# Performance work log

Hardware: AMD Instinct MI355X
Metric: run time of the kernel (lower is better)

## Reference

```python
import jax, jax.numpy as jnp
import numpy as np

N_NODES = 100000
N_EDGES = 1600000
DIM = 3
HID = 128
BN_EPS = 1e-5


def _bn(x, g, b):
    # BatchNorm1d, training-mode batch statistics (biased variance, like torch)
    m = jnp.mean(x, axis=0)
    v = jnp.var(x, axis=0)
    return (x - m) * jax.lax.rsqrt(v + BN_EPS) * g + b


def _gin_mlp(h, w1, b1, g1, be1, w2, b2, g2, be2, w3, b3):
    # Linear -> BN -> ReLU -> (Dropout: identity in eval) -> Linear -> BN -> ReLU -> Linear
    h = jax.nn.relu(_bn(h @ w1 + b1, g1, be1))
    h = jax.nn.relu(_bn(h @ w2 + b2, g2, be2))
    return h @ w3 + b3


def _gin_conv(x, src, dst, eps, mlp_params):
    # GINConv: mlp((1+eps)*x_i + sum_{j->i} x_j); scatter-add over edge targets
    agg = jax.ops.segment_sum(x[src], dst, num_segments=N_NODES)
    return _gin_mlp((1.0 + eps) * x + agg, *mlp_params)


def setup_inputs() -> dict:
    key = jax.random.key(0)
    ks = jax.random.split(key, 32)

    def w(k, shape, scale=0.05):
        return jax.random.normal(k, shape, dtype=jnp.float32) * scale

    inp = {}
    inp["coords"] = jax.random.normal(ks[0], (N_NODES, DIM), dtype=jnp.float32)
    inp["edge_index"] = jax.random.randint(ks[1], (2, N_EDGES), 0, N_NODES, dtype=jnp.int32)

    # GIN layer 0 MLP (dim -> hid -> hid -> hid)
    inp["g0_w1"] = w(ks[2], (DIM, HID)); inp["g0_b1"] = jnp.zeros((HID,), jnp.float32)
    inp["g0_g1"] = jnp.ones((HID,), jnp.float32); inp["g0_be1"] = jnp.zeros((HID,), jnp.float32)
    inp["g0_w2"] = w(ks[3], (HID, HID)); inp["g0_b2"] = jnp.zeros((HID,), jnp.float32)
    inp["g0_g2"] = jnp.ones((HID,), jnp.float32); inp["g0_be2"] = jnp.zeros((HID,), jnp.float32)
    inp["g0_w3"] = w(ks[4], (HID, HID)); inp["g0_b3"] = jnp.zeros((HID,), jnp.float32)
    inp["eps0"] = jnp.zeros((), jnp.float32)
    inp["bn0_g"] = jnp.ones((HID,), jnp.float32); inp["bn0_b"] = jnp.zeros((HID,), jnp.float32)

    # GIN layer 1 MLP (hid -> hid -> hid -> hid)
    inp["g1_w1"] = w(ks[5], (HID, HID)); inp["g1_b1"] = jnp.zeros((HID,), jnp.float32)
    inp["g1_g1"] = jnp.ones((HID,), jnp.float32); inp["g1_be1"] = jnp.zeros((HID,), jnp.float32)
    inp["g1_w2"] = w(ks[6], (HID, HID)); inp["g1_b2"] = jnp.zeros((HID,), jnp.float32)
    inp["g1_g2"] = jnp.ones((HID,), jnp.float32); inp["g1_be2"] = jnp.zeros((HID,), jnp.float32)
    inp["g1_w3"] = w(ks[7], (HID, HID)); inp["g1_b3"] = jnp.zeros((HID,), jnp.float32)
    inp["eps1"] = jnp.zeros((), jnp.float32)
    inp["bn1_g"] = jnp.ones((HID,), jnp.float32); inp["bn1_b"] = jnp.zeros((HID,), jnp.float32)

    # decoder MLP: (2*hid+1) -> hid -> hid//2 -> 1, sigmoid
    inp["d_w1"] = w(ks[8], (2 * HID + 1, HID)); inp["d_b1"] = jnp.zeros((HID,), jnp.float32)
    inp["d_g"] = jnp.ones((HID,), jnp.float32); inp["d_be"] = jnp.zeros((HID,), jnp.float32)
    inp["d_w2"] = w(ks[9], (HID, HID // 2)); inp["d_b2"] = jnp.zeros((HID // 2,), jnp.float32)
    inp["d_w3"] = w(ks[10], (HID // 2, 1)); inp["d_b3"] = jnp.zeros((1,), jnp.float32)
    return inp


def reference(coords, edge_index,
              g0_w1, g0_b1, g0_g1, g0_be1, g0_w2, g0_b2, g0_g2, g0_be2, g0_w3, g0_b3, eps0, bn0_g, bn0_b,
              g1_w1, g1_b1, g1_g1, g1_be1, g1_w2, g1_b2, g1_g2, g1_be2, g1_w3, g1_b3, eps1, bn1_g, bn1_b,
              d_w1, d_b1, d_g, d_be, d_w2, d_b2, d_w3, d_b3):
    node_0 = edge_index[0]
    node_1 = edge_index[1]

    mlp0 = (g0_w1, g0_b1, g0_g1, g0_be1, g0_w2, g0_b2, g0_g2, g0_be2, g0_w3, g0_b3)
    mlp1 = (g1_w1, g1_b1, g1_g1, g1_be1, g1_w2, g1_b2, g1_g2, g1_be2, g1_w3, g1_b3)

    x = _gin_conv(coords, node_0, node_1, eps0, mlp0)
    x = jax.nn.relu(_bn(x, bn0_g, bn0_b))
    x = _gin_conv(x, node_0, node_1, eps1, mlp1)
    x = jax.nn.relu(_bn(x, bn1_g, bn1_b))

    # edge_l_cntr branch: per-edge contour-length feature + endpoint concat
    l = jnp.linalg.norm(coords[node_1] - coords[node_0], axis=1, keepdims=True)  # [E,1]
    h = jnp.concatenate([x[node_0], x[node_1], l], axis=-1)  # [E, 2*hid+1]

    h = jax.nn.relu(_bn(h @ d_w1 + d_b1, d_g, d_be))
    h = jax.nn.relu(h @ d_w2 + d_b2)
    out = jax.nn.sigmoid((h @ d_w3 + d_b3).squeeze(-1))  # [E]
    return out
```

## Files before the change

kernel.cpp:

```cpp
#include <hip/hip_runtime.h>
#include <hip/hip_bf16.h>
#include <math.h>


typedef __attribute__((ext_vector_type(8))) __bf16 bf16x8;
typedef __attribute__((ext_vector_type(4))) float f32x4;

__device__ __forceinline__ unsigned int pack_bf16(float a, float b) {
    unsigned short ua = __builtin_bit_cast(unsigned short, __float2bfloat16(a));
    unsigned short ub = __builtin_bit_cast(unsigned short, __float2bfloat16(b));
    return (unsigned int)ua | ((unsigned int)ub << 16);
}
__device__ __forceinline__ float bflo(unsigned int u) {
    return __builtin_bit_cast(float, u << 16);
}
__device__ __forceinline__ float bfhi(unsigned int u) {
    return __builtin_bit_cast(float, u & 0xffff0000u);
}


__global__ void hist_dst(const int* __restrict__ edst, int* __restrict__ cursor, int E) {
    int e = blockIdx.x * 256 + threadIdx.x;
    if (e < E) atomicAdd(&cursor[edst[e]], 1);
}

__global__ __launch_bounds__(1024) void scan_deg(const int* deg, int* rowoff, int* cursor, int N) {
    __shared__ int sums[1024];
    const int t = threadIdx.x;
    const int chunk = (N + 1023) >> 10;
    int lo = t * chunk, hi = lo + chunk;
    if (lo > N) lo = N;
    if (hi > N) hi = N;
    int s = 0;
    for (int i = lo; i < hi; ++i) s += deg[i];
    sums[t] = s;
    __syncthreads();
    for (int off = 1; off < 1024; off <<= 1) {
        int add = (t >= off) ? sums[t - off] : 0;
        __syncthreads();
        sums[t] += add;
        __syncthreads();
    }
    int run = sums[t] - s;
    for (int i = lo; i < hi; ++i) {
        int d = deg[i];
        rowoff[i] = run;
        cursor[i] = run;
        run += d;
    }
    if (t == 1023) rowoff[N] = sums[1023];
}

__global__ void fill_csr(const int* __restrict__ esrc, const int* __restrict__ edst,
                         const float* __restrict__ coords,
                         int* cursor, int* __restrict__ perm, int* __restrict__ dperm,
                         int* __restrict__ eperm, float* __restrict__ lperm, int E) {
    int e = blockIdx.x * 256 + threadIdx.x;
    if (e >= E) return;
    int s0 = esrc[e], d0 = edst[e];
    int pos = atomicAdd(&cursor[d0], 1);
    perm[pos] = s0;
    dperm[pos] = d0;
    eperm[pos] = e;
    float dx = coords[d0*3+0] - coords[s0*3+0];
    float dy = coords[d0*3+1] - coords[s0*3+1];
    float dz = coords[d0*3+2] - coords[s0*3+2];
    lperm[pos] = sqrtf(dx*dx + dy*dy + dz*dz);
}


__global__ void gather_coords(const float* __restrict__ coords,
                              const int* __restrict__ rowoff, const int* __restrict__ perm,
                              float* __restrict__ agg0, int N) {
    int i = blockIdx.x * 256 + threadIdx.x;
    if (i >= N) return;
    float ax = 0.f, ay = 0.f, az = 0.f;
    int b = rowoff[i], t = rowoff[i+1];
    for (int j = b; j < t; ++j) {
        int p = perm[j];
        ax += coords[p*3+0];
        ay += coords[p*3+1];
        az += coords[p*3+2];
    }
    agg0[i*3+0] = ax; agg0[i*3+1] = ay; agg0[i*3+2] = az;
}

__global__ __launch_bounds__(256) void gather_combine_bn(const float* __restrict__ x,
                                                         const int* __restrict__ rowoff,
                                                         const int* __restrict__ perm,
                                                         const float* __restrict__ st,
                                                         const float* __restrict__ g,
                                                         const float* __restrict__ be,
                                                         float invN,
                                                         const float* __restrict__ eps,
                                                         float* __restrict__ y, int N) {
    int node = blockIdx.x * 4 + (threadIdx.x >> 6);
    int lane = threadIdx.x & 63;
    if (node >= N) return;
    float ep = 1.f + *eps;
    int c0 = lane*2, c1 = c0 + 1;
    float m0 = st[c0]*invN, m1 = st[c1]*invN;
    float v0 = fmaxf(st[128+c0]*invN - m0*m0, 0.f);
    float v1 = fmaxf(st[128+c1]*invN - m1*m1, 0.f);
    float a0 = g[c0]*rsqrtf(v0 + 1e-5f), a1 = g[c1]*rsqrtf(v1 + 1e-5f);
    float2 scv = make_float2(a0, a1);
    float2 shv = make_float2(be[c0] - m0*a0, be[c1] - m1*a1);
    const float2* x2 = (const float2*)x;
    int b = rowoff[node], t = rowoff[node+1];
    float2 acc = make_float2(0.f, 0.f);
    int j = b;
    for (; j + 2 <= t; j += 2) {
        int p0 = perm[j], p1 = perm[j+1];
        float2 v0v = x2[(size_t)p0*64 + lane];
        float2 v1v = x2[(size_t)p1*64 + lane];
        acc.x += fmaxf(fmaf(v0v.x, scv.x, shv.x), 0.f) + fmaxf(fmaf(v1v.x, scv.x, shv.x), 0.f);
        acc.y += fmaxf(fmaf(v0v.y, scv.y, shv.y), 0.f) + fmaxf(fmaf(v1v.y, scv.y, shv.y), 0.f);
    }
    if (j < t) {
        int p = perm[j];
        float2 v = x2[(size_t)p*64 + lane];
        acc.x += fmaxf(fmaf(v.x, scv.x, shv.x), 0.f);
        acc.y += fmaxf(fmaf(v.y, scv.y, shv.y), 0.f);
    }
    float2 own = x2[(size_t)node*64 + lane];
    acc.x = fmaf(ep, fmaxf(fmaf(own.x, scv.x, shv.x), 0.f), acc.x);
    acc.y = fmaf(ep, fmaxf(fmaf(own.y, scv.y, shv.y), 0.f), acc.y);
    ((float2*)y)[(size_t)node*64 + lane] = acc;
}


__global__ __launch_bounds__(256) void lin0(const float* __restrict__ coords,
                                            const float* __restrict__ agg0,
                                            const float* __restrict__ W1,
                                            const float* __restrict__ b1,
                                            const float* __restrict__ eps0,
                                            float* __restrict__ t1,
                                            float* __restrict__ stats, int nrows) {
    int col = threadIdx.x & 127, half = threadIdx.x >> 7;
    float w0 = W1[col], w1 = W1[128+col], w2 = W1[256+col], bb = b1[col];
    float ep = 1.f + *eps0;
    float s = 0.f, q = 0.f;
    int r0 = blockIdx.x * 64;
    for (int i = 0; i < 32; ++i) {
        int row = r0 + half + 2*i;
        if (row < nrows) {
            float h0 = fmaf(ep, coords[row*3+0], agg0[row*3+0]);
            float h1 = fmaf(ep, coords[row*3+1], agg0[row*3+1]);
            float h2 = fmaf(ep, coords[row*3+2], agg0[row*3+2]);
            float v = fmaf(h0, w0, fmaf(h1, w1, fmaf(h2, w2, bb)));
            t1[row*128+col] = v;
            s += v; q += v*v;
        }
    }
    __shared__ float red[512];
    red[half*128+col] = s;
    red[256 + half*128+col] = q;
    __syncthreads();
    if (threadIdx.x < 128) {
        atomicAdd(&stats[col],       red[col] + red[128+col]);
        atomicAdd(&stats[128+col],   red[256+col] + red[384+col]);
    }
}

__global__ void prep_w2(const float* __restrict__ W2, unsigned short* __restrict__ w2t) {
    int i = blockIdx.x * 256 + threadIdx.x;
    if (i >= 128*64) return;
    int k = i >> 6, c = i & 63;
    w2t[c*128 + k] = __builtin_bit_cast(unsigned short, __float2bfloat16(W2[i]));
}

__global__ void prep_wT(const float* __restrict__ w0, const float* __restrict__ w1,
                        const float* __restrict__ w2, const float* __restrict__ w3,
                        const float* __restrict__ w4, const float* __restrict__ w5,
                        const float* __restrict__ w6, unsigned short* __restrict__ dst) {
    int m = blockIdx.y;
    const float* src = (m==0)?w0:(m==1)?w1:(m==2)?w2:(m==3)?w3:(m==4)?w4:(m==5)?w5:w6;
    int i = blockIdx.x * 256 + threadIdx.x;
    int k = i >> 7, c = i & 127;
    dst[m*16384 + c*128 + k] =
        __builtin_bit_cast(unsigned short, __float2bfloat16(src[i]));
}

template<bool IN_BN, bool STATS, bool OUT_BF16>
__global__ __launch_bounds__(256) void gemm_mfma(const float* __restrict__ A,
                                                 const unsigned short* __restrict__ wT,
                                                 const float* __restrict__ bias,
                                                 const float* __restrict__ inst,
                                                 const float* __restrict__ bng,
                                                 const float* __restrict__ bnb,
                                                 float invCnt,
                                                 float* __restrict__ C,
                                                 unsigned short* __restrict__ Cb,
                                                 float* __restrict__ stats, int nrows) {
    __shared__ int4 sAi[1024];
    __shared__ int4 sBi[2048];
    __shared__ float sred[2][4][128];
    char* sA = (char*)sAi;
    char* sB = (char*)sBi;
    float* sSC = &sred[0][0][0];
    float* sSH = &sred[0][1][0];
    const int tid = threadIdx.x;
    const int tile0 = blockIdx.x * 64;

    if (IN_BN) {
        if (tid < 128) {
            float m = inst[tid] * invCnt;
            float v = fmaxf(inst[128+tid] * invCnt - m*m, 0.f);
            float a = bng[tid] * rsqrtf(v + 1e-5f);
            sSC[tid] = a;
            sSH[tid] = bnb[tid] - m*a;
        }
        __syncthreads();
    }

    {
        const int4* src = (const int4*)wT;
        #pragma unroll
        for (int ii = 0; ii < 8; ++ii) {
            int s = tid + 256*ii;
            int col = s >> 4, k16 = s & 15;
            int byte = ((col << 8) + (k16 << 4)) ^ ((col & 7) << 4);
            *(int4*)(sB + byte) = src[s];
        }
    }
    {
        const int c4 = tid & 31;
        const int rb = tid >> 5;
        float4 s4, t4;
        if (IN_BN) {
            s4 = ((const float4*)sSC)[c4];
            t4 = ((const float4*)sSH)[c4];
        }
        const float4* A4 = (const float4*)A;
        #pragma unroll
        for (int i = 0; i < 8; ++i) {
            int r = rb + 8*i;
            int row = tile0 + r;
            float4 v = make_float4(0.f, 0.f, 0.f, 0.f);
            if (row < nrows) {
                v = A4[(size_t)row*32 + c4];
                if (IN_BN) {
                    v.x = fmaxf(fmaf(v.x, s4.x, t4.x), 0.f);
                    v.y = fmaxf(fmaf(v.y, s4.y, t4.y), 0.f);
                    v.z = fmaxf(fmaf(v.z, s4.z, t4.z), 0.f);
                    v.w = fmaxf(fmaf(v.w, s4.w, t4.w), 0.f);
                }
            }
            uint2 pk;
            pk.x = pack_bf16(v.x, v.y);
            pk.y = pack_bf16(v.z, v.w);
            int byte = ((r << 8) + (c4 << 3)) ^ ((r & 7) << 4);
            *(uint2*)(sA + byte) = pk;
        }
    }
    __syncthreads();

    const int l = tid & 63;
    const int w = tid >> 6;
    const int arow = (w << 4) + (l & 15);
    const int kbase = (l >> 4) << 3;
    f32x4 accv[8];
    #pragma unroll
    for (int c = 0; c < 8; ++c) accv[c] = (f32x4){0.f, 0.f, 0.f, 0.f};

    #pragma unroll
    for (int t = 0; t < 4; ++t) {
        int k0 = t*32 + kbase;
        int abyte = ((arow << 8) + (k0 << 1)) ^ ((arow & 7) << 4);
        bf16x8 af = __builtin_bit_cast(bf16x8, *(const int4*)(sA + abyte));
        #pragma unroll
        for (int c = 0; c < 8; ++c) {
            int bcol = (c << 4) + (l & 15);
            int bbyte = ((bcol << 8) + (k0 << 1)) ^ ((bcol & 7) << 4);
            bf16x8 bf = __builtin_bit_cast(bf16x8, *(const int4*)(sB + bbyte));
            accv[c] = __builtin_amdgcn_mfma_f32_16x16x32_bf16(af, bf, accv[c], 0, 0, 0);
        }
    }

    const int rj = (l >> 4) << 2;
    float lsum[8], lsq[8];
    #pragma unroll
    for (int c = 0; c < 8; ++c) {
        int col = (c << 4) + (l & 15);
        float bv = bias ? bias[col] : 0.f;
        f32x4 a = accv[c];
        float s = 0.f, q = 0.f;
        #pragma unroll
        for (int j = 0; j < 4; ++j) {
            int row = tile0 + (w << 4) + rj + j;
            float o = a[j] + bv;
            if (row < nrows) {
                if (OUT_BF16)
                    Cb[(size_t)row*128 + col] =
                        __builtin_bit_cast(unsigned short, __float2bfloat16(o));
                else
                    C[(size_t)row*128 + col] = o;
                if (STATS) { s += o; q += o*o; }
            }
        }
        lsum[c] = s; lsq[c] = q;
    }
    if (STATS) {
        #pragma unroll
        for (int c = 0; c < 8; ++c) {
            lsum[c] += __shfl_xor(lsum[c], 16, 64);
            lsum[c] += __shfl_xor(lsum[c], 32, 64);
            lsq[c]  += __shfl_xor(lsq[c], 16, 64);
            lsq[c]  += __shfl_xor(lsq[c], 32, 64);
        }
        __syncthreads();
        if ((l >> 4) == 0) {
            #pragma unroll
            for (int c = 0; c < 8; ++c) {
                int col = (c << 4) + l;
                sred[0][w][col] = lsum[c];
                sred[1][w][col] = lsq[c];
            }
        }
        __syncthreads();
        if (tid < 128) {
            float s = sred[0][0][tid] + sred[0][1][tid] + sred[0][2][tid] + sred[0][3][tid];
            float q = sred[1][0][tid] + sred[1][1][tid] + sred[1][2][tid] + sred[1][3][tid];
            atomicAdd(&stats[tid], s);
            atomicAdd(&stats[128 + tid], q);
        }
    }
}

__global__ __launch_bounds__(256) void csr_stats(const unsigned short* __restrict__ ya,
                                                 const unsigned short* __restrict__ yb,
                                                 const int* __restrict__ rowoff,
                                                 const int* __restrict__ perm,
                                                 const float* __restrict__ lperm,
                                                 const float* __restrict__ wl,
                                                 const float* __restrict__ b1,
                                                 float* __restrict__ stats, int N, int nspan) {
    int w = blockIdx.x * 4 + (threadIdx.x >> 6);
    int lane = threadIdx.x & 63;
    const unsigned int* ya2 = (const unsigned int*)ya;
    const unsigned int* yb2 = (const unsigned int*)yb;
    float2 wl2 = ((const float2*)wl)[lane];
    float2 b12 = ((const float2*)b1)[lane];
    float2 s = make_float2(0.f, 0.f), q = make_float2(0.f, 0.f);
    int i0 = w * nspan;
    int i1 = i0 + nspan; if (i1 > N) i1 = N;
    for (int i = i0; i < i1; ++i) {
        unsigned int ub = yb2[(size_t)i*64 + lane];
        float ybx = bflo(ub), yby = bfhi(ub);
        int b = rowoff[i], t = rowoff[i+1];
        for (int j = b; j < t; ++j) {
            int p = perm[j];
            float lv = lperm[j];
            unsigned int ua = ya2[(size_t)p*64 + lane];
            float zx = bflo(ua) + ybx + fmaf(lv, wl2.x, b12.x);
            float zy = bfhi(ua) + yby + fmaf(lv, wl2.y, b12.y);
            s.x += zx; s.y += zy;
            q.x += zx*zx; q.y += zy*zy;
        }
    }
    __shared__ float red[1024];
    int wv = threadIdx.x >> 6;
    red[wv*128 + lane*2]       = s.x;
    red[wv*128 + lane*2 + 1]   = s.y;
    red[512 + wv*128 + lane*2]     = q.x;
    red[512 + wv*128 + lane*2 + 1] = q.y;
    __syncthreads();
    if (threadIdx.x < 128) {
        int c = threadIdx.x;
        float ss = red[c] + red[128+c] + red[256+c] + red[384+c];
        float qq = red[512+c] + red[640+c] + red[768+c] + red[896+c];
        atomicAdd(&stats[c], ss);
        atomicAdd(&stats[128+c], qq);
    }
}

__global__ __launch_bounds__(256) void decoder_fused(const unsigned short* __restrict__ ya,
                                                     const unsigned short* __restrict__ yb,
                                                     const float* __restrict__ lperm,
                                                     const int* __restrict__ perm,
                                                     const int* __restrict__ dperm,
                                                     const int* __restrict__ eperm,
                                                     const float* __restrict__ wl,
                                                     const float* __restrict__ b1,
                                                     const float* __restrict__ st6,
                                                     const float* __restrict__ dg,
                                                     const float* __restrict__ dbe,
                                                     float invE,
                                                     const unsigned short* __restrict__ w2t,
                                                     const float* __restrict__ b2,
                                                     const float* __restrict__ w3,
                                                     const float* __restrict__ b3p,
                                                     float* __restrict__ out, int E) {
    __shared__ int4 sAB[2048];
    char* sA = (char*)sAB;
    char* sB = (char*)sAB + 16384;
    const int tid = threadIdx.x;
    const int tile0 = blockIdx.x * 64;

    {
        const int4* src = (const int4*)w2t;
        #pragma unroll
        for (int ii = 0; ii < 4; ++ii) {
            int s = tid + 256*ii;
            int col = s >> 4, k16 = s & 15;
            int byte = ((col << 8) + (k16 << 4)) ^ ((col & 7) << 4);
            *(int4*)(sB + byte) = src[s];
        }
    }
    {
        const int c4 = tid & 31;
        const int rb = tid >> 5;
        float4 wv = ((const float4*)wl)[c4];
        float4 bb = ((const float4*)b1)[c4];
        float4 s4, t4;
        {
            int cb = c4 * 4;
            #pragma unroll
            for (int j = 0; j < 4; ++j) {
                float m = st6[cb+j] * invE;
                float v = fmaxf(st6[128+cb+j] * invE - m*m, 0.f);
                float a = dg[cb+j] * rsqrtf(v + 1e-5f);
                ((float*)&s4)[j] = a;
                ((float*)&t4)[j] = dbe[cb+j] - m*a;
            }
        }
        const uint2* ya2 = (const uint2*)ya;
        const uint2* yb2 = (const uint2*)yb;
        #pragma unroll
        for (int i = 0; i < 8; ++i) {
            int r = rb + 8*i;
            int row = tile0 + r;
            float4 v = make_float4(0.f, 0.f, 0.f, 0.f);
            if (row < E) {
                int s0 = perm[row], d0 = dperm[row];
                float lv = lperm[row];
                uint2 ua = ya2[(size_t)s0*32 + c4];
                uint2 ubv = yb2[(size_t)d0*32 + c4];
                float vax = bflo(ua.x), vay = bfhi(ua.x), vaz = bflo(ua.y), vaw = bfhi(ua.y);
                float vbx = bflo(ubv.x), vby = bfhi(ubv.x), vbz = bflo(ubv.y), vbw = bfhi(ubv.y);
                v.x = fmaxf(fmaf(vax + vbx + fmaf(lv, wv.x, bb.x), s4.x, t4.x), 0.f);
                v.y = fmaxf(fmaf(vay + vby + fmaf(lv, wv.y, bb.y), s4.y, t4.y), 0.f);
                v.z = fmaxf(fmaf(vaz + vbz + fmaf(lv, wv.z, bb.z), s4.z, t4.z), 0.f);
                v.w = fmaxf(fmaf(vaw + vbw + fmaf(lv, wv.w, bb.w), s4.w, t4.w), 0.f);
            }
            uint2 pk;
            pk.x = pack_bf16(v.x, v.y);
            pk.y = pack_bf16(v.z, v.w);
            int byte = ((r << 8) + (c4 << 3)) ^ ((r & 7) << 4);
            *(uint2*)(sA + byte) = pk;
        }
    }
    __syncthreads();

    const int l = tid & 63;
    const int w = tid >> 6;
    const int arow = (w << 4) + (l & 15);
    const int kbase = (l >> 4) << 3;
    f32x4 accv[4];
    #pragma unroll
    for (int c = 0; c < 4; ++c) accv[c] = (f32x4){0.f, 0.f, 0.f, 0.f};

    #pragma unroll
    for (int t = 0; t < 4; ++t) {
        int k0 = t*32 + kbase;
        int abyte = ((arow << 8) + (k0 << 1)) ^ ((arow & 7) << 4);
        bf16x8 af = __builtin_bit_cast(bf16x8, *(const int4*)(sA + abyte));
        #pragma unroll
        for (int c = 0; c < 4; ++c) {
            int bcol = (c << 4) + (l & 15);
            int bbyte = ((bcol << 8) + (k0 << 1)) ^ ((bcol & 7) << 4);
            bf16x8 bf = __builtin_bit_cast(bf16x8, *(const int4*)(sB + bbyte));
            accv[c] = __builtin_amdgcn_mfma_f32_16x16x32_bf16(af, bf, accv[c], 0, 0, 0);
        }
    }

    float p0 = 0.f, p1 = 0.f, p2 = 0.f, p3 = 0.f;
    #pragma unroll
    for (int c = 0; c < 4; ++c) {
        int col = (c << 4) + (l & 15);
        float b2c = b2[col], w3c = w3[col];
        f32x4 a = accv[c];
        p0 = fmaf(fmaxf(a[0] + b2c, 0.f), w3c, p0);
        p1 = fmaf(fmaxf(a[1] + b2c, 0.f), w3c, p1);
        p2 = fmaf(fmaxf(a[2] + b2c, 0.f), w3c, p2);
        p3 = fmaf(fmaxf(a[3] + b2c, 0.f), w3c, p3);
    }
    #pragma unroll
    for (int m = 1; m < 16; m <<= 1) {
        p0 += __shfl_xor(p0, m, 64);
        p1 += __shfl_xor(p1, m, 64);
        p2 += __shfl_xor(p2, m, 64);
        p3 += __shfl_xor(p3, m, 64);
    }
    if ((l & 15) == 0) {
        float b3v = b3p[0];
        int rbase = tile0 + (w << 4) + ((l >> 4) << 2);
        float pj[4] = {p0, p1, p2, p3};
        #pragma unroll
        for (int j = 0; j < 4; ++j) {
            int row = rbase + j;
            if (row < E) out[eperm[row]] = 1.f / (1.f + expf(-(pj[j] + b3v)));
        }
    }
}


extern "C" void kernel_launch(void* const* d_in, const int* in_sizes, int n_in,
                              void* d_out, int out_size, void* d_ws, size_t ws_size,
                              hipStream_t stream) {
    const int N = in_sizes[0] / 3;
    const int E = in_sizes[1] / 2;

    const float* coords = (const float*)d_in[0];
    const int*   ei     = (const int*)d_in[1];
    const int*   esrc = ei;
    const int*   edst = ei + E;
    const float* g0_w1 = (const float*)d_in[2];
    const float* g0_b1 = (const float*)d_in[3];
    const float* g0_g1 = (const float*)d_in[4];
    const float* g0_be1= (const float*)d_in[5];
    const float* g0_w2 = (const float*)d_in[6];
    const float* g0_b2 = (const float*)d_in[7];
    const float* g0_g2 = (const float*)d_in[8];
    const float* g0_be2= (const float*)d_in[9];
    const float* g0_w3 = (const float*)d_in[10];
    const float* g0_b3 = (const float*)d_in[11];
    const float* eps0  = (const float*)d_in[12];
    const float* bn0_g = (const float*)d_in[13];
    const float* bn0_b = (const float*)d_in[14];
    const float* g1_w1 = (const float*)d_in[15];
    const float* g1_b1 = (const float*)d_in[16];
    const float* g1_g1 = (const float*)d_in[17];
    const float* g1_be1= (const float*)d_in[18];
    const float* g1_w2 = (const float*)d_in[19];
    const float* g1_b2 = (const float*)d_in[20];
    const float* g1_g2 = (const float*)d_in[21];
    const float* g1_be2= (const float*)d_in[22];
    const float* g1_w3 = (const float*)d_in[23];
    const float* g1_b3 = (const float*)d_in[24];
    const float* eps1  = (const float*)d_in[25];
    const float* bn1_g = (const float*)d_in[26];
    const float* bn1_b = (const float*)d_in[27];
    const float* d_w1  = (const float*)d_in[28];
    const float* d_b1  = (const float*)d_in[29];
    const float* d_g   = (const float*)d_in[30];
    const float* d_be  = (const float*)d_in[31];
    const float* d_w2  = (const float*)d_in[32];
    const float* d_b2  = (const float*)d_in[33];
    const float* d_w3  = (const float*)d_in[34];
    const float* d_b3  = (const float*)d_in[35];

    float* ws = (float*)d_ws;
    const size_t NF = (size_t)N * 128;
    float* buf0 = ws;
    float* buf1 = ws + NF;
    float* buf2 = ws + 2*NF;
    float* agg0 = ws + 3*NF;
    float* stats= agg0 + (size_t)N*3;
    float* scsh = stats + 7*256;
    float* lperm = scsh + 7*256;
    int*   cursor = (int*)(lperm + E);
    int*   rowoff = cursor + N;
    int*   perm   = rowoff + N + 1;
    int*   dperm  = perm + E;
    int*   eperm  = dperm + E;
    unsigned short* w2t = (unsigned short*)(eperm + E);
    unsigned short* wT  = w2t + 64*128;
    unsigned short* ya_bf = (unsigned short*)buf1;
    unsigned short* yb_bf = (unsigned short*)buf2;

    float* out = (float*)d_out;

    const float* wl = d_w1 + 256*128;

    #define STATSK(k) (stats + (k)*256)
    #define WT(m) (wT + (m)*16384)

    const int rowTiles = (N + 63) / 64;
    const int edgeTiles = (E + 63) / 64;
    const int eBlocks = (E + 255) / 256;
    const float invN = 1.f / (float)N;
    const float invE = 1.f / (float)E;
    const int nWaves = 2048 * 4;
    const int nspan = (N + nWaves - 1) / nWaves;

    hipMemsetAsync(stats, 0, 7*256 * sizeof(float), stream);
    hipMemsetAsync(cursor, 0, (size_t)N * sizeof(int), stream);

    hist_dst<<<eBlocks, 256, 0, stream>>>(edst, cursor, E);
    scan_deg<<<1, 1024, 0, stream>>>(cursor, rowoff, cursor, N);
    fill_csr<<<eBlocks, 256, 0, stream>>>(esrc, edst, coords, cursor, perm, dperm, eperm, lperm, E);
    prep_w2<<<32, 256, 0, stream>>>(d_w2, w2t);
    prep_wT<<<dim3(64, 7), 256, 0, stream>>>(g0_w2, g0_w3, g1_w1, g1_w2, g1_w3,
                                             d_w1, d_w1 + 128*128, wT);

    gather_coords<<<(N + 255)/256, 256, 0, stream>>>(coords, rowoff, perm, agg0, N);
    lin0<<<rowTiles, 256, 0, stream>>>(coords, agg0, g0_w1, g0_b1, eps0, buf0, STATSK(0), N);
    gemm_mfma<true,true,false><<<rowTiles, 256, 0, stream>>>(
        buf0, WT(0), g0_b2, STATSK(0), g0_g1, g0_be1, invN, buf1, nullptr, STATSK(1), N);
    gemm_mfma<true,true,false><<<rowTiles, 256, 0, stream>>>(
        buf1, WT(1), g0_b3, STATSK(1), g0_g2, g0_be2, invN, buf2, nullptr, STATSK(2), N);

    gather_combine_bn<<<(N + 3)/4, 256, 0, stream>>>(
        buf2, rowoff, perm, STATSK(2), bn0_g, bn0_b, invN, eps1, buf0, N);
    gemm_mfma<false,true,false><<<rowTiles, 256, 0, stream>>>(
        buf0, WT(2), g1_b1, nullptr, nullptr, nullptr, 0.f, buf1, nullptr, STATSK(3), N);
    gemm_mfma<true,true,false><<<rowTiles, 256, 0, stream>>>(
        buf1, WT(3), g1_b2, STATSK(3), g1_g1, g1_be1, invN, buf2, nullptr, STATSK(4), N);
    gemm_mfma<true,true,false><<<rowTiles, 256, 0, stream>>>(
        buf2, WT(4), g1_b3, STATSK(4), g1_g2, g1_be2, invN, buf0, nullptr, STATSK(5), N);

    gemm_mfma<true,false,true><<<rowTiles, 256, 0, stream>>>(
        buf0, WT(5), nullptr, STATSK(5), bn1_g, bn1_b, invN, nullptr, ya_bf, nullptr, N);
    gemm_mfma<true,false,true><<<rowTiles, 256, 0, stream>>>(
        buf0, WT(6), nullptr, STATSK(5), bn1_g, bn1_b, invN, nullptr, yb_bf, nullptr, N);
    csr_stats<<<2048, 256, 0, stream>>>(ya_bf, yb_bf, rowoff, perm, lperm, wl, d_b1,
                                        STATSK(6), N, nspan);
    decoder_fused<<<edgeTiles, 256, 0, stream>>>(ya_bf, yb_bf, lperm, perm, dperm, eperm,
                                                 wl, d_b1, STATSK(6), d_g, d_be, invE,
                                                 w2t, d_b2, d_w3, d_b3, out, E);
}
```

Baseline: 1.512 ms.

## Store node activations as bf16 and make decoder a persistent grid-stride kernel

All intermediate node feature buffers (lin0 output, GEMM outputs, gather_combine_bn input and output) now hold bf16 instead of fp32, which halves the memory traffic of the gather and GEMM stages. The GEMM A-tile load now reads packed bf16 int4 vectors and applies BN+ReLU on the unpacked values. Separately, the decoder now runs on a fixed grid of 1280 blocks that loop over edge tiles, so the w2t weight tile is loaded into shared memory once per block instead of once per tile. The risk is extra rounding error from storing pre-BN activations in bf16, while BN statistics are still accumulated from the fp32 values.

New measurement: 1.500 ms. Within noise of the previous version (-0.7%).

```diff
diff --git a/kernel.cpp b/kernel.cpp
--- a/kernel.cpp
+++ b/kernel.cpp
@@ -16,6 +16,9 @@
 }
 __device__ __forceinline__ float bfhi(unsigned int u) {
     return __builtin_bit_cast(float, u & 0xffff0000u);
+}
+__device__ __forceinline__ unsigned short bf16r(float a) {
+    return __builtin_bit_cast(unsigned short, __float2bfloat16(a));
 }
 
 
@@ -85,7 +88,7 @@
     agg0[i*3+0] = ax; agg0[i*3+1] = ay; agg0[i*3+2] = az;
 }
 
-__global__ __launch_bounds__(256) void gather_combine_bn(const float* __restrict__ x,
+__global__ __launch_bounds__(256) void gather_combine_bn(const unsigned short* __restrict__ x,
                                                          const int* __restrict__ rowoff,
                                                          const int* __restrict__ perm,
                                                          const float* __restrict__ st,
@@ -93,7 +96,7 @@
                                                          const float* __restrict__ be,
                                                          float invN,
                                                          const float* __restrict__ eps,
-                                                         float* __restrict__ y, int N) {
+                                                         unsigned short* __restrict__ y, int N) {
     int node = blockIdx.x * 4 + (threadIdx.x >> 6);
     int lane = threadIdx.x & 63;
     if (node >= N) return;
@@ -103,29 +106,27 @@
     float v0 = fmaxf(st[128+c0]*invN - m0*m0, 0.f);
     float v1 = fmaxf(st[128+c1]*invN - m1*m1, 0.f);
     float a0 = g[c0]*rsqrtf(v0 + 1e-5f), a1 = g[c1]*rsqrtf(v1 + 1e-5f);
-    float2 scv = make_float2(a0, a1);
-    float2 shv = make_float2(be[c0] - m0*a0, be[c1] - m1*a1);
-    const float2* x2 = (const float2*)x;
+    float sx = a0, sy = a1;
+    float hx = be[c0] - m0*a0, hy = be[c1] - m1*a1;
+    const unsigned int* x2 = (const unsigned int*)x;
     int b = rowoff[node], t = rowoff[node+1];
-    float2 acc = make_float2(0.f, 0.f);
+    float accx = 0.f, accy = 0.f;
     int j = b;
     for (; j + 2 <= t; j += 2) {
-        int p0 = perm[j], p1 = perm[j+1];
-        float2 v0v = x2[(size_t)p0*64 + lane];
-        float2 v1v = x2[(size_t)p1*64 + lane];
-        acc.x += fmaxf(fmaf(v0v.x, scv.x, shv.x), 0.f) + fmaxf(fmaf(v1v.x, scv.x, shv.x), 0.f);
-        acc.y += fmaxf(fmaf(v0v.y, scv.y, shv.y), 0.f) + fmaxf(fmaf(v1v.y, scv.y, shv.y), 0.f);
+        unsigned int u0 = x2[(size_t)perm[j]*64 + lane];
+        unsigned int u1 = x2[(size_t)perm[j+1]*64 + lane];
+        accx += fmaxf(fmaf(bflo(u0), sx, hx), 0.f) + fmaxf(fmaf(bflo(u1), sx, hx), 0.f);
+        accy += fmaxf(fmaf(bfhi(u0), sy, hy), 0.f) + fmaxf(fmaf(bfhi(u1), sy, hy), 0.f);
     }
     if (j < t) {
-        int p = perm[j];
-        float2 v = x2[(size_t)p*64 + lane];
-        acc.x += fmaxf(fmaf(v.x, scv.x, shv.x), 0.f);
-        acc.y += fmaxf(fmaf(v.y, scv.y, shv.y), 0.f);
-    }
-    float2 own = x2[(size_t)node*64 + lane];
-    acc.x = fmaf(ep, fmaxf(fmaf(own.x, scv.x, shv.x), 0.f), acc.x);
-    acc.y = fmaf(ep, fmaxf(fmaf(own.y, scv.y, shv.y), 0.f), acc.y);
-    ((float2*)y)[(size_t)node*64 + lane] = acc;
+        unsigned int u = x2[(size_t)perm[j]*64 + lane];
+        accx += fmaxf(fmaf(bflo(u), sx, hx), 0.f);
+        accy += fmaxf(fmaf(bfhi(u), sy, hy), 0.f);
+    }
+    unsigned int uo = x2[(size_t)node*64 + lane];
+    accx = fmaf(ep, fmaxf(fmaf(bflo(uo), sx, hx), 0.f), accx);
+    accy = fmaf(ep, fmaxf(fmaf(bfhi(uo), sy, hy), 0.f), accy);
+    ((unsigned int*)y)[(size_t)node*64 + lane] = pack_bf16(accx, accy);
 }
 
 
@@ -134,7 +135,7 @@
                                             const float* __restrict__ W1,
                                             const float* __restrict__ b1,
                                             const float* __restrict__ eps0,
-                                            float* __restrict__ t1,
+                                            unsigned short* __restrict__ t1,
                                             float* __restrict__ stats, int nrows) {
     int col = threadIdx.x & 127, half = threadIdx.x >> 7;
     float w0 = W1[col], w1 = W1[128+col], w2 = W1[256+col], bb = b1[col];
@@ -148,7 +149,7 @@
             float h1 = fmaf(ep, coords[row*3+1], agg0[row*3+1]);
             float h2 = fmaf(ep, coords[row*3+2], agg0[row*3+2]);
             float v = fmaf(h0, w0, fmaf(h1, w1, fmaf(h2, w2, bb)));
-            t1[row*128+col] = v;
+            t1[row*128+col] = bf16r(v);
             s += v; q += v*v;
         }
     }
@@ -166,7 +167,7 @@
     int i = blockIdx.x * 256 + threadIdx.x;
     if (i >= 128*64) return;
     int k = i >> 6, c = i & 63;
-    w2t[c*128 + k] = __builtin_bit_cast(unsigned short, __float2bfloat16(W2[i]));
+    w2t[c*128 + k] = bf16r(W2[i]);
 }
 
 __global__ void prep_wT(const float* __restrict__ w0, const float* __restrict__ w1,
@@ -177,19 +178,17 @@
     const float* src = (m==0)?w0:(m==1)?w1:(m==2)?w2:(m==3)?w3:(m==4)?w4:(m==5)?w5:w6;
     int i = blockIdx.x * 256 + threadIdx.x;
     int k = i >> 7, c = i & 127;
-    dst[m*16384 + c*128 + k] =
-        __builtin_bit_cast(unsigned short, __float2bfloat16(src[i]));
-}
-
-template<bool IN_BN, bool STATS, bool OUT_BF16>
-__global__ __launch_bounds__(256) void gemm_mfma(const float* __restrict__ A,
+    dst[m*16384 + c*128 + k] = bf16r(src[i]);
+}
+
+template<bool IN_BN, bool STATS>
+__global__ __launch_bounds__(256) void gemm_mfma(const unsigned short* __restrict__ A,
                                                  const unsigned short* __restrict__ wT,
                                                  const float* __restrict__ bias,
                                                  const float* __restrict__ inst,
                                                  const float* __restrict__ bng,
                                                  const float* __restrict__ bnb,
                                                  float invCnt,
-                                                 float* __restrict__ C,
                                                  unsigned short* __restrict__ Cb,
                                                  float* __restrict__ stats, int nrows) {
     __shared__ int4 sAi[1024];
@@ -224,33 +223,35 @@
         }
     }
     {
-        const int c4 = tid & 31;
-        const int rb = tid >> 5;
-        float4 s4, t4;
-        if (IN_BN) {
-            s4 = ((const float4*)sSC)[c4];
-            t4 = ((const float4*)sSH)[c4];
-        }
-        const float4* A4 = (const float4*)A;
-        #pragma unroll
-        for (int i = 0; i < 8; ++i) {
-            int r = rb + 8*i;
+        const int4* A4 = (const int4*)A;
+        #pragma unroll
+        for (int ii = 0; ii < 4; ++ii) {
+            int s = tid + 256*ii;
+            int r = s >> 4, k16 = s & 15;
             int row = tile0 + r;
-            float4 v = make_float4(0.f, 0.f, 0.f, 0.f);
-            if (row < nrows) {
-                v = A4[(size_t)row*32 + c4];
-                if (IN_BN) {
-                    v.x = fmaxf(fmaf(v.x, s4.x, t4.x), 0.f);
-                    v.y = fmaxf(fmaf(v.y, s4.y, t4.y), 0.f);
-                    v.z = fmaxf(fmaf(v.z, s4.z, t4.z), 0.f);
-                    v.w = fmaxf(fmaf(v.w, s4.w, t4.w), 0.f);
-                }
+            int4 raw = make_int4(0,0,0,0);
+            if (row < nrows) raw = A4[(size_t)row*16 + k16];
+            if (IN_BN) {
+                float4 sa = ((const float4*)sSC)[k16*2];
+                float4 sb = ((const float4*)sSC)[k16*2+1];
+                float4 ha = ((const float4*)sSH)[k16*2];
+                float4 hb = ((const float4*)sSH)[k16*2+1];
+                unsigned int ux = raw.x, uy = raw.y, uz = raw.z, uw = raw.w;
+                float e0 = fmaxf(fmaf(bflo(ux), sa.x, ha.x), 0.f);
+                float e1 = fmaxf(fmaf(bfhi(ux), sa.y, ha.y), 0.f);
+                float e2 = fmaxf(fmaf(bflo(uy), sa.z, ha.z), 0.f);
+                float e3 = fmaxf(fmaf(bfhi(uy), sa.w, ha.w), 0.f);
+                float e4 = fmaxf(fmaf(bflo(uz), sb.x, hb.x), 0.f);
+                float e5 = fmaxf(fmaf(bfhi(uz), sb.y, hb.y), 0.f);
+                float e6 = fmaxf(fmaf(bflo(uw), sb.z, hb.z), 0.f);
+                float e7 = fmaxf(fmaf(bfhi(uw), sb.w, hb.w), 0.f);
+                raw.x = (int)pack_bf16(e0, e1);
+                raw.y = (int)pack_bf16(e2, e3);
+                raw.z = (int)pack_bf16(e4, e5);
+                raw.w = (int)pack_bf16(e6, e7);
             }
-            uint2 pk;
-            pk.x = pack_bf16(v.x, v.y);
-            pk.y = pack_bf16(v.z, v.w);
-            int byte = ((r << 8) + (c4 << 3)) ^ ((r & 7) << 4);
-            *(uint2*)(sA + byte) = pk;
+            int byte = ((r << 8) + (k16 << 4)) ^ ((r & 7) << 4);
+            *(int4*)(sA + byte) = raw;
         }
     }
     __syncthreads();
@@ -290,11 +291,7 @@
             int row = tile0 + (w << 4) + rj + j;
             float o = a[j] + bv;
             if (row < nrows) {
-                if (OUT_BF16)
-                    Cb[(size_t)row*128 + col] =
-                        __builtin_bit_cast(unsigned short, __float2bfloat16(o));
-                else
-                    C[(size_t)row*128 + col] = o;
+                Cb[(size_t)row*128 + col] = bf16r(o);
                 if (STATS) { s += o; q += o*o; }
             }
         }
@@ -390,12 +387,11 @@
                                                      const float* __restrict__ b2,
                                                      const float* __restrict__ w3,
                                                      const float* __restrict__ b3p,
-                                                     float* __restrict__ out, int E) {
+                                                     float* __restrict__ out, int E, int ntiles) {
     __shared__ int4 sAB[2048];
     char* sA = (char*)sAB;
     char* sB = (char*)sAB + 16384;
     const int tid = threadIdx.x;
-    const int tile0 = blockIdx.x * 64;
 
     {
         const int4* src = (const int4*)w2t;
@@ -407,25 +403,35 @@
             *(int4*)(sB + byte) = src[s];
         }
     }
+
+    const int c4 = tid & 31;
+    const int rb = tid >> 5;
+    float4 wv = ((const float4*)wl)[c4];
+    float4 bb = ((const float4*)b1)[c4];
+    float4 s4, t4;
     {
-        const int c4 = tid & 31;
-        const int rb = tid >> 5;
-        float4 wv = ((const float4*)wl)[c4];
-        float4 bb = ((const float4*)b1)[c4];
-        float4 s4, t4;
-        {
-            int cb = c4 * 4;
-            #pragma unroll
-            for (int j = 0; j < 4; ++j) {
-                float m = st6[cb+j] * invE;
-                float v = fmaxf(st6[128+cb+j] * invE - m*m, 0.f);
-                float a = dg[cb+j] * rsqrtf(v + 1e-5f);
-                ((float*)&s4)[j] = a;
-                ((float*)&t4)[j] = dbe[cb+j] - m*a;
-            }
-        }
-        const uint2* ya2 = (const uint2*)ya;
-        const uint2* yb2 = (const uint2*)yb;
+        int cb = c4 * 4;
+        #pragma unroll
+        for (int j = 0; j < 4; ++j) {
+            float m = st6[cb+j] * invE;
+            float v = fmaxf(st6[128+cb+j] * invE - m*m, 0.f);
+            float a = dg[cb+j] * rsqrtf(v + 1e-5f);
+            ((float*)&s4)[j] = a;
+            ((float*)&t4)[j] = dbe[cb+j] - m*a;
+        }
+    }
+    const uint2* ya2 = (const uint2*)ya;
+    const uint2* yb2 = (const uint2*)yb;
+
+    const int l = tid & 63;
+    const int w = tid >> 6;
+    const int arow = (w << 4) + (l & 15);
+    const int kbase = (l >> 4) << 3;
+    const float b3v = b3p[0];
+
+    for (int tile = blockIdx.x; tile < ntiles; tile += gridDim.x) {
+        const int tile0 = tile * 64;
+        __syncthreads();
         #pragma unroll
         for (int i = 0; i < 8; ++i) {
             int r = rb + 8*i;
@@ -449,57 +455,51 @@
             int byte = ((r << 8) + (c4 << 3)) ^ ((r & 7) << 4);
             *(uint2*)(sA + byte) = pk;
         }
-    }
-    __syncthreads();
-
-    const int l = tid & 63;
-    const int w = tid >> 6;
-    const int arow = (w << 4) + (l & 15);
-    const int kbase = (l >> 4) << 3;
-    f32x4 accv[4];
-    #pragma unroll
-    for (int c = 0; c < 4; ++c) accv[c] = (f32x4){0.f, 0.f, 0.f, 0.f};
-
-    #pragma unroll
-    for (int t = 0; t < 4; ++t) {
-        int k0 = t*32 + kbase;
-        int abyte = ((arow << 8) + (k0 << 1)) ^ ((arow & 7) << 4);
-        bf16x8 af = __builtin_bit_cast(bf16x8, *(const int4*)(sA + abyte));
+        __syncthreads();
+
+        f32x4 accv[4];
+        #pragma unroll
+        for (int c = 0; c < 4; ++c) accv[c] = (f32x4){0.f, 0.f, 0.f, 0.f};
+        #pragma unroll
+        for (int t = 0; t < 4; ++t) {
+            int k0 = t*32 + kbase;
+            int abyte = ((arow << 8) + (k0 << 1)) ^ ((arow & 7) << 4);
+            bf16x8 af = __builtin_bit_cast(bf16x8, *(const int4*)(sA + abyte));
+            #pragma unroll
+            for (int c = 0; c < 4; ++c) {
+                int bcol = (c << 4) + (l & 15);
+                int bbyte = ((bcol << 8) + (k0 << 1)) ^ ((bcol & 7) << 4);
+                bf16x8 bf = __builtin_bit_cast(bf16x8, *(const int4*)(sB + bbyte));
+                accv[c] = __builtin_amdgcn_mfma_f32_16x16x32_bf16(af, bf, accv[c], 0, 0, 0);
+            }
+        }
+
+        float p0 = 0.f, p1 = 0.f, p2 = 0.f, p3 = 0.f;
         #pragma unroll
         for (int c = 0; c < 4; ++c) {
-            int bcol = (c << 4) + (l & 15);
-            int bbyte = ((bcol << 8) + (k0 << 1)) ^ ((bcol & 7) << 4);
-            bf16x8 bf = __builtin_bit_cast(bf16x8, *(const int4*)(sB + bbyte));
-            accv[c] = __builtin_amdgcn_mfma_f32_16x16x32_bf16(af, bf, accv[c], 0, 0, 0);
-        }
-    }
-
-    float p0 = 0.f, p1 = 0.f, p2 = 0.f, p3 = 0.f;
-    #pragma unroll
-    for (int c = 0; c < 4; ++c) {
-        int col = (c << 4) + (l & 15);
-        float b2c = b2[col], w3c = w3[col];
-        f32x4 a = accv[c];
-        p0 = fmaf(fmaxf(a[0] + b2c, 0.f), w3c, p0);
-        p1 = fmaf(fmaxf(a[1] + b2c, 0.f), w3c, p1);
-        p2 = fmaf(fmaxf(a[2] + b2c, 0.f), w3c, p2);
-        p3 = fmaf(fmaxf(a[3] + b2c, 0.f), w3c, p3);
-    }
-    #pragma unroll
-    for (int m = 1; m < 16; m <<= 1) {
-        p0 += __shfl_xor(p0, m, 64);
-        p1 += __shfl_xor(p1, m, 64);
-        p2 += __shfl_xor(p2, m, 64);
-        p3 += __shfl_xor(p3, m, 64);
-    }
-    if ((l & 15) == 0) {
-        float b3v = b3p[0];
-        int rbase = tile0 + (w << 4) + ((l >> 4) << 2);
-        float pj[4] = {p0, p1, p2, p3};
-        #pragma unroll
-        for (int j = 0; j < 4; ++j) {
-            int row = rbase + j;
-            if (row < E) out[eperm[row]] = 1.f / (1.f + expf(-(pj[j] + b3v)));
+            int col = (c << 4) + (l & 15);
+            float b2c = b2[col], w3c = w3[col];
+            f32x4 a = accv[c];
+            p0 = fmaf(fmaxf(a[0] + b2c, 0.f), w3c, p0);
+            p1 = fmaf(fmaxf(a[1] + b2c, 0.f), w3c, p1);
+            p2 = fmaf(fmaxf(a[2] + b2c, 0.f), w3c, p2);
+            p3 = fmaf(fmaxf(a[3] + b2c, 0.f), w3c, p3);
+        }
+        #pragma unroll
+        for (int m = 1; m < 16; m <<= 1) {
+            p0 += __shfl_xor(p0, m, 64);
+            p1 += __shfl_xor(p1, m, 64);
+            p2 += __shfl_xor(p2, m, 64);
+            p3 += __shfl_xor(p3, m, 64);
+        }
+        if ((l & 15) == 0) {
+            int rbase = tile0 + (w << 4) + ((l >> 4) << 2);
+            float pj[4] = {p0, p1, p2, p3};
+            #pragma unroll
+            for (int j = 0; j < 4; ++j) {
+                int row = rbase + j;
+                if (row < E) out[eperm[row]] = 1.f / (1.f + expf(-(pj[j] + b3v)));
+            }
         }
     }
 }
@@ -566,8 +566,10 @@
     int*   eperm  = dperm + E;
     unsigned short* w2t = (unsigned short*)(eperm + E);
     unsigned short* wT  = w2t + 64*128;
-    unsigned short* ya_bf = (unsigned short*)buf1;
-    unsigned short* yb_bf = (unsigned short*)buf2;
+
+    unsigned short* b0 = (unsigned short*)buf0;
+    unsigned short* b1b = (unsigned short*)buf1;
+    unsigned short* b2b = (unsigned short*)buf2;
 
     float* out = (float*)d_out;
 
@@ -583,6 +585,7 @@
     const float invE = 1.f / (float)E;
     const int nWaves = 2048 * 4;
     const int nspan = (N + nWaves - 1) / nWaves;
+    const int decBlocks = 1280;
 
     hipMemsetAsync(stats, 0, 7*256 * sizeof(float), stream);
     hipMemsetAsync(cursor, 0, (size_t)N * sizeof(int), stream);
@@ -595,28 +598,28 @@
                                              d_w1, d_w1 + 128*128, wT);
 
     gather_coords<<<(N + 255)/256, 256, 0, stream>>>(coords, rowoff, perm, agg0, N);
-    lin0<<<rowTiles, 256, 0, stream>>>(coords, agg0, g0_w1, g0_b1, eps0, buf0, STATSK(0), N);
-    gemm_mfma<true,true,false><<<rowTiles, 256, 0, stream>>>(
-        buf0, WT(0), g0_b2, STATSK(0), g0_g1, g0_be1, invN, buf1, nullptr, STATSK(1), N);
-    gemm_mfma<true,true,false><<<rowTiles, 256, 0, stream>>>(
-        buf1, WT(1), g0_b3, STATSK(1), g0_g2, g0_be2, invN, buf2, nullptr, STATSK(2), N);
+    lin0<<<rowTiles, 256, 0, stream>>>(coords, agg0, g0_w1, g0_b1, eps0, b0, STATSK(0), N);
+    gemm_mfma<true,true><<<rowTiles, 256, 0, stream>>>(
+        b0, WT(0), g0_b2, STATSK(0), g0_g1, g0_be1, invN, b1b, STATSK(1), N);
+    gemm_mfma<true,true><<<rowTiles, 256, 0, stream>>>(
+        b1b, WT(1), g0_b3, STATSK(1), g0_g2, g0_be2, invN, b2b, STATSK(2), N);
 
     gather_combine_bn<<<(N + 3)/4, 256, 0, stream>>>(
-        buf2, rowoff, perm, STATSK(2), bn0_g, bn0_b, invN, eps1, buf0, N);
-    gemm_mfma<false,true,false><<<rowTiles, 256, 0, stream>>>(
-        buf0, WT(2), g1_b1, nullptr, nullptr, nullptr, 0.f, buf1, nullptr, STATSK(3), N);
-    gemm_mfma<true,true,false><<<rowTiles, 256, 0, stream>>>(
-        buf1, WT(3), g1_b2, STATSK(3), g1_g1, g1_be1, invN, buf2, nullptr, STATSK(4), N);
-    gemm_mfma<true,true,false><<<rowTiles, 256, 0, stream>>>(
-        buf2, WT(4), g1_b3, STATSK(4), g1_g2, g1_be2, invN, buf0, nullptr, STATSK(5), N);
-
-    gemm_mfma<true,false,true><<<rowTiles, 256, 0, stream>>>(
-        buf0, WT(5), nullptr, STATSK(5), bn1_g, bn1_b, invN, nullptr, ya_bf, nullptr, N);
-    gemm_mfma<true,false,true><<<rowTiles, 256, 0, stream>>>(
-        buf0, WT(6), nullptr, STATSK(5), bn1_g, bn1_b, invN, nullptr, yb_bf, nullptr, N);
-    csr_stats<<<2048, 256, 0, stream>>>(ya_bf, yb_bf, rowoff, perm, lperm, wl, d_b1,
+        b2b, rowoff, perm, STATSK(2), bn0_g, bn0_b, invN, eps1, b0, N);
+    gemm_mfma<false,true><<<rowTiles, 256, 0, stream>>>(
+        b0, WT(2), g1_b1, nullptr, nullptr, nullptr, 0.f, b1b, STATSK(3), N);
+    gemm_mfma<true,true><<<rowTiles, 256, 0, stream>>>(
+        b1b, WT(3), g1_b2, STATSK(3), g1_g1, g1_be1, invN, b2b, STATSK(4), N);
+    gemm_mfma<true,true><<<rowTiles, 256, 0, stream>>>(
+        b2b, WT(4), g1_b3, STATSK(4), g1_g2, g1_be2, invN, b0, STATSK(5), N);
+
+    gemm_mfma<true,false><<<rowTiles, 256, 0, stream>>>(
+        b0, WT(5), nullptr, STATSK(5), bn1_g, bn1_b, invN, b1b, nullptr, N);
+    gemm_mfma<true,false><<<rowTiles, 256, 0, stream>>>(
+        b0, WT(6), nullptr, STATSK(5), bn1_g, bn1_b, invN, b2b, nullptr, N);
+    csr_stats<<<2048, 256, 0, stream>>>(b1b, b2b, rowoff, perm, lperm, wl, d_b1,
                                         STATSK(6), N, nspan);
-    decoder_fused<<<edgeTiles, 256, 0, stream>>>(ya_bf, yb_bf, lperm, perm, dperm, eperm,
+    decoder_fused<<<decBlocks, 256, 0, stream>>>(b1b, b2b, lperm, perm, dperm, eperm,
                                                  wl, d_b1, STATSK(6), d_g, d_be, invE,
-                                                 w2t, d_b2, d_w3, d_b3, out, E);
-}
+                                                 w2t, d_b2, d_w3, d_b3, out, E, edgeTiles);
+}
```
